# Optimization experiments

Measured on AMD Instinct MI355X. Metric: run time of the kernel, lower is better.

The kernel has to match this reference:

```python
import jax, jax.numpy as jnp
import numpy as np

B, S, SIZE = 2048, 512, 96  # size = embedding_size(32) * num_feature(3)


def setup_inputs() -> dict:
    key = jax.random.key(0)
    k1, k2, k3, k4, k5, k6, k7 = jax.random.split(key, 7)
    bound = 1.0 / np.sqrt(SIZE)  # nn.Linear default init range
    return {
        "seq_item_embedding": jax.random.normal(k1, (B, S, SIZE), dtype=jnp.float32),
        "target_item_embedding": jax.random.normal(k2, (B, 1, SIZE), dtype=jnp.float32),
        "mask": jax.random.randint(k3, (B, S + 1, 1), 0, 2).astype(jnp.bool_),
        "w1_weight": jax.random.uniform(k4, (SIZE, SIZE), jnp.float32, -bound, bound),
        "w1_bias": jax.random.uniform(k5, (SIZE,), jnp.float32, -bound, bound),
        "w2_weight": jax.random.uniform(k6, (SIZE, SIZE), jnp.float32, -bound, bound),
        "w2_bias": jax.random.uniform(k7, (SIZE,), jnp.float32, -bound, bound),
    }


def reference(seq_item_embedding, target_item_embedding, mask,
              w1_weight, w1_bias, w2_weight, w2_bias):
    # mask[:, :-1, :] -> [B, S] boolean (True = masked out)
    m = mask[:, :-1, 0]
    # w1(seq): [B, S, size]; note source reassigns seq_item_embedding to this,
    # so the final weighted pool uses the projected sequence.
    seq_h = jnp.einsum('bsd,ed->bse', seq_item_embedding, w1_weight) + w1_bias
    # w2(target): [B, 1, size], broadcasts over seq_len (repeat in torch)
    tgt_h = jnp.einsum('bqd,ed->bqe', target_item_embedding, w2_weight) + w2_bias
    # sigmoid(sum) reduced over feature dim -> scores [B, S]
    scores = jax.nn.sigmoid(seq_h + tgt_h).sum(axis=-1)
    scores = jnp.where(m, jnp.float32(-1e9), scores)
    attn = jax.nn.softmax(scores, axis=-1)  # [B, S]
    # weighted pool over seq dim -> [B, size]
    output = jnp.einsum('bs,bse->be', attn, seq_h)
    return output
```

## Files before the change

kernel.cpp:

```cpp
#include <hip/hip_runtime.h>
#include <hip/hip_bf16.h>
#include <math.h>

#define NB 2048
#define NS 512
#define ND 96
#define SH_STRIDE 112

typedef __attribute__((ext_vector_type(8))) short short8;
typedef __attribute__((ext_vector_type(4))) float floatx4;

__device__ __forceinline__ short f2bf(float f) {
    union { float f; unsigned u; } c; c.f = f;
    unsigned u = c.u;
    u += 0x7FFF + ((u >> 16) & 1);
    return (short)(u >> 16);
}
__device__ __forceinline__ float bf2f(short s) {
    union { unsigned u; float f; } c;
    c.u = ((unsigned)(unsigned short)s) << 16;
    return c.f;
}

__global__ __launch_bounds__(256, 1)
void attn_fused(const float* __restrict__ seq,
                const float* __restrict__ tgt,
                const int*   __restrict__ mask,
                const float* __restrict__ w1,
                const float* __restrict__ b1,
                const float* __restrict__ w2,
                const float* __restrict__ b2,
                float* __restrict__ out)
{
    __shared__ short sh[NS * SH_STRIDE];
    __shared__ float sc_lds[NS];
    __shared__ float attn[NS];
    __shared__ float tgt_h[ND];
    __shared__ float red[8];
    __shared__ float osum[2][ND];

    const int b    = blockIdx.x;
    const int tid  = threadIdx.x;
    const int lane = tid & 63;
    const int wave = tid >> 6;
    const int l15  = lane & 15;
    const int quad = lane >> 4;

    if (tid < ND) {
        const float* tv = tgt + (size_t)b * ND;
        const float* wr = w2 + tid * ND;
        float acc = b2[tid];
        #pragma unroll
        for (int d = 0; d < ND; d += 4) {
            acc += tv[d]*wr[d] + tv[d+1]*wr[d+1] + tv[d+2]*wr[d+2] + tv[d+3]*wr[d+3];
        }
        tgt_h[tid] = acc;
    }

    short8 bfrag[6][3];
    float biasv[6];
    #pragma unroll
    for (int t = 0; t < 6; ++t) {
        const int e = 16 * t + l15;
        biasv[t] = b1[e];
        #pragma unroll
        for (int kk = 0; kk < 3; ++kk) {
            const float* p = w1 + e * ND + kk * 32 + quad * 8;
            floatx4 p0 = *(const floatx4*)(p);
            floatx4 p1 = *(const floatx4*)(p + 4);
            short8 v;
            v[0]=f2bf(p0[0]); v[1]=f2bf(p0[1]); v[2]=f2bf(p0[2]); v[3]=f2bf(p0[3]);
            v[4]=f2bf(p1[0]); v[5]=f2bf(p1[1]); v[6]=f2bf(p1[2]); v[7]=f2bf(p1[3]);
            bfrag[t][kk] = v;
        }
    }

    __syncthreads();

    float tgtv[6];
    #pragma unroll
    for (int t = 0; t < 6; ++t) tgtv[t] = tgt_h[16 * t + l15];

    const float* abase = seq + ((size_t)b * NS + l15) * ND + quad * 8;

    #pragma unroll
    for (int sti = 0; sti < 8; ++sti) {
        const int st = wave * 8 + sti;
        const int s0 = st * 16;
        short8 af[3];
        #pragma unroll
        for (int kk = 0; kk < 3; ++kk) {
            const float* p = abase + (size_t)s0 * ND + kk * 32;
            floatx4 p0 = *(const floatx4*)(p);
            floatx4 p1 = *(const floatx4*)(p + 4);
            short8 v;
            v[0]=f2bf(p0[0]); v[1]=f2bf(p0[1]); v[2]=f2bf(p0[2]); v[3]=f2bf(p0[3]);
            v[4]=f2bf(p1[0]); v[5]=f2bf(p1[1]); v[6]=f2bf(p1[2]); v[7]=f2bf(p1[3]);
            af[kk] = v;
        }
        float part0 = 0.f, part1 = 0.f, part2 = 0.f, part3 = 0.f;
        #pragma unroll
        for (int t = 0; t < 6; ++t) {
            floatx4 acc = { biasv[t], biasv[t], biasv[t], biasv[t] };
            acc = __builtin_amdgcn_mfma_f32_16x16x32_bf16(af[0], bfrag[t][0], acc, 0, 0, 0);
            acc = __builtin_amdgcn_mfma_f32_16x16x32_bf16(af[1], bfrag[t][1], acc, 0, 0, 0);
            acc = __builtin_amdgcn_mfma_f32_16x16x32_bf16(af[2], bfrag[t][2], acc, 0, 0, 0);
            const int e = 16 * t + l15;
            short* dst = &sh[(s0 + quad * 4) * SH_STRIDE + e];
            const float x0 = acc[0], x1 = acc[1], x2 = acc[2], x3 = acc[3];
            dst[0]             = f2bf(x0);
            dst[SH_STRIDE]     = f2bf(x1);
            dst[2 * SH_STRIDE] = f2bf(x2);
            dst[3 * SH_STRIDE] = f2bf(x3);
            const float th = tgtv[t];
            part0 += 1.0f / (1.0f + __expf(-(x0 + th)));
            part1 += 1.0f / (1.0f + __expf(-(x1 + th)));
            part2 += 1.0f / (1.0f + __expf(-(x2 + th)));
            part3 += 1.0f / (1.0f + __expf(-(x3 + th)));
        }
        #pragma unroll
        for (int off = 1; off < 16; off <<= 1) {
            part0 += __shfl_xor(part0, off, 64);
            part1 += __shfl_xor(part1, off, 64);
            part2 += __shfl_xor(part2, off, 64);
            part3 += __shfl_xor(part3, off, 64);
        }
        if (l15 == 0) {
            sc_lds[s0 + quad * 4 + 0] = part0;
            sc_lds[s0 + quad * 4 + 1] = part1;
            sc_lds[s0 + quad * 4 + 2] = part2;
            sc_lds[s0 + quad * 4 + 3] = part3;
        }
    }
    __syncthreads();

    float v0 = sc_lds[tid];
    float v1 = sc_lds[tid + 256];
    if (mask[(size_t)b * (NS + 1) + tid] != 0)       v0 = -1e9f;
    if (mask[(size_t)b * (NS + 1) + tid + 256] != 0) v1 = -1e9f;
    float mx = fmaxf(v0, v1);
    #pragma unroll
    for (int off = 1; off < 64; off <<= 1) mx = fmaxf(mx, __shfl_xor(mx, off, 64));
    if (lane == 0) red[wave] = mx;
    __syncthreads();
    mx = fmaxf(fmaxf(red[0], red[1]), fmaxf(red[2], red[3]));
    const float e0 = __expf(v0 - mx);
    const float e1 = __expf(v1 - mx);
    float ssum = e0 + e1;
    #pragma unroll
    for (int off = 1; off < 64; off <<= 1) ssum += __shfl_xor(ssum, off, 64);
    if (lane == 0) red[4 + wave] = ssum;
    __syncthreads();
    const float inv = 1.0f / (red[4] + red[5] + red[6] + red[7]);
    attn[tid]       = e0 * inv;
    attn[tid + 256] = e1 * inv;
    __syncthreads();

    if (tid < 2 * ND) {
        const int half = tid / ND;
        const int e    = tid - half * ND;
        float acc = 0.f;
        const int sb = half * 256;
        #pragma unroll 4
        for (int s = sb; s < sb + 256; ++s) {
            acc += attn[s] * bf2f(sh[s * SH_STRIDE + e]);
        }
        osum[half][e] = acc;
    }
    __syncthreads();
    if (tid < ND) out[(size_t)b * ND + tid] = osum[0][tid] + osum[1][tid];
}

extern "C" void kernel_launch(void* const* d_in, const int* in_sizes, int n_in,
                              void* d_out, int out_size, void* d_ws, size_t ws_size,
                              hipStream_t stream) {
    const float* seq  = (const float*)d_in[0];
    const float* tgt  = (const float*)d_in[1];
    const int*   mask = (const int*)d_in[2];
    const float* w1   = (const float*)d_in[3];
    const float* b1   = (const float*)d_in[4];
    const float* w2   = (const float*)d_in[5];
    const float* b2   = (const float*)d_in[6];
    float* out = (float*)d_out;
    attn_fused<<<dim3(NB), dim3(256), 0, stream>>>(seq, tgt, mask, w1, b1, w2, b2, out);
}
```

Before: 637.8 us.

## Keep projected sequence in registers, stage W1 fragments in LDS, use 512 threads

The projected sequence is no longer written to a large bf16 LDS buffer (about 114KB, which allowed one block per CU). Each lane now keeps its MFMA outputs packed as bf16 pairs in registers and computes the weighted pool directly from them, using cross-quad shuffles and a per-wave LDS reduction. The W1 bf16 fragments move from per-thread registers into a small shared LDS table, and the block grows to 512 threads with launch bounds (512,4), so several blocks can be resident per CU for better latency hiding. The cost is extra LDS reads of W1 inside the MFMA loop and higher register pressure from the packed outputs.

Result: faster. 589.7 us (-7.5%).

```diff
diff --git a/kernel.cpp b/kernel.cpp
--- a/kernel.cpp
+++ b/kernel.cpp
@@ -1,28 +1,33 @@
 #include <hip/hip_runtime.h>
-#include <hip/hip_bf16.h>
 #include <math.h>
 
 #define NB 2048
 #define NS 512
 #define ND 96
-#define SH_STRIDE 112
 
 typedef __attribute__((ext_vector_type(8))) short short8;
 typedef __attribute__((ext_vector_type(4))) float floatx4;
 
-__device__ __forceinline__ short f2bf(float f) {
+__device__ __forceinline__ unsigned f2bfu(float f) {
     union { float f; unsigned u; } c; c.f = f;
     unsigned u = c.u;
     u += 0x7FFF + ((u >> 16) & 1);
-    return (short)(u >> 16);
-}
-__device__ __forceinline__ float bf2f(short s) {
-    union { unsigned u; float f; } c;
-    c.u = ((unsigned)(unsigned short)s) << 16;
-    return c.f;
-}
-
-__global__ __launch_bounds__(256, 1)
+    return u >> 16;
+}
+__device__ __forceinline__ unsigned pack2(float a, float b) {
+    return f2bfu(a) | (f2bfu(b) << 16);
+}
+__device__ __forceinline__ float lo_f(unsigned u) {
+    union { unsigned u; float f; } c; c.u = u << 16; return c.f;
+}
+__device__ __forceinline__ float hi_f(unsigned u) {
+    union { unsigned u; float f; } c; c.u = u & 0xFFFF0000u; return c.f;
+}
+__device__ __forceinline__ float sigm(float x) {
+    return 1.0f / (1.0f + __expf(-x));
+}
+
+__global__ __launch_bounds__(512, 4)
 void attn_fused(const float* __restrict__ seq,
                 const float* __restrict__ tgt,
                 const int*   __restrict__ mask,
@@ -32,12 +37,12 @@
                 const float* __restrict__ b2,
                 float* __restrict__ out)
 {
-    __shared__ short sh[NS * SH_STRIDE];
-    __shared__ float sc_lds[NS];
-    __shared__ float attn[NS];
-    __shared__ float tgt_h[ND];
-    __shared__ float red[8];
-    __shared__ float osum[2][ND];
+    __shared__ short w1f[18 * 64 * 8];
+    __shared__ float sc[NS];
+    __shared__ float at[NS];
+    __shared__ float th[ND];
+    __shared__ float red1[8], red2[8];
+    __shared__ float osum[8][ND];
 
     const int b    = blockIdx.x;
     const int tid  = threadIdx.x;
@@ -46,6 +51,23 @@
     const int l15  = lane & 15;
     const int quad = lane >> 4;
 
+    for (int idx = tid; idx < 1152; idx += 512) {
+        const int e  = idx / 12;
+        const int dc = idx - 12 * e;
+        const int kk = dc >> 2;
+        const int q  = dc & 3;
+        const float* p = w1 + e * ND + kk * 32 + q * 8;
+        floatx4 p0 = *(const floatx4*)(p);
+        floatx4 p1 = *(const floatx4*)(p + 4);
+        short8 v;
+        v[0]=(short)f2bfu(p0[0]); v[1]=(short)f2bfu(p0[1]);
+        v[2]=(short)f2bfu(p0[2]); v[3]=(short)f2bfu(p0[3]);
+        v[4]=(short)f2bfu(p1[0]); v[5]=(short)f2bfu(p1[1]);
+        v[6]=(short)f2bfu(p1[2]); v[7]=(short)f2bfu(p1[3]);
+        const int t = e >> 4, r = e & 15;
+        *(short8*)&w1f[(((t * 3 + kk) * 64) + q * 16 + r) * 8] = v;
+    }
+
     if (tid < ND) {
         const float* tv = tgt + (size_t)b * ND;
         const float* wr = w2 + tid * ND;
@@ -54,39 +76,23 @@
         for (int d = 0; d < ND; d += 4) {
             acc += tv[d]*wr[d] + tv[d+1]*wr[d+1] + tv[d+2]*wr[d+2] + tv[d+3]*wr[d+3];
         }
-        tgt_h[tid] = acc;
-    }
-
-    short8 bfrag[6][3];
-    float biasv[6];
+        th[tid] = acc;
+    }
+    __syncthreads();
+
+    float tgtv[6], biasv[6];
     #pragma unroll
     for (int t = 0; t < 6; ++t) {
-        const int e = 16 * t + l15;
-        biasv[t] = b1[e];
-        #pragma unroll
-        for (int kk = 0; kk < 3; ++kk) {
-            const float* p = w1 + e * ND + kk * 32 + quad * 8;
-            floatx4 p0 = *(const floatx4*)(p);
-            floatx4 p1 = *(const floatx4*)(p + 4);
-            short8 v;
-            v[0]=f2bf(p0[0]); v[1]=f2bf(p0[1]); v[2]=f2bf(p0[2]); v[3]=f2bf(p0[3]);
-            v[4]=f2bf(p1[0]); v[5]=f2bf(p1[1]); v[6]=f2bf(p1[2]); v[7]=f2bf(p1[3]);
-            bfrag[t][kk] = v;
-        }
-    }
-
-    __syncthreads();
-
-    float tgtv[6];
-    #pragma unroll
-    for (int t = 0; t < 6; ++t) tgtv[t] = tgt_h[16 * t + l15];
-
+        tgtv[t]  = th[16 * t + l15];
+        biasv[t] = b1[16 * t + l15];
+    }
+
+    unsigned pk[4][6][2];
     const float* abase = seq + ((size_t)b * NS + l15) * ND + quad * 8;
 
     #pragma unroll
-    for (int sti = 0; sti < 8; ++sti) {
-        const int st = wave * 8 + sti;
-        const int s0 = st * 16;
+    for (int sti = 0; sti < 4; ++sti) {
+        const int s0 = (wave * 4 + sti) * 16;
         short8 af[3];
         #pragma unroll
         for (int kk = 0; kk < 3; ++kk) {
@@ -94,81 +100,95 @@
             floatx4 p0 = *(const floatx4*)(p);
             floatx4 p1 = *(const floatx4*)(p + 4);
             short8 v;
-            v[0]=f2bf(p0[0]); v[1]=f2bf(p0[1]); v[2]=f2bf(p0[2]); v[3]=f2bf(p0[3]);
-            v[4]=f2bf(p1[0]); v[5]=f2bf(p1[1]); v[6]=f2bf(p1[2]); v[7]=f2bf(p1[3]);
+            v[0]=(short)f2bfu(p0[0]); v[1]=(short)f2bfu(p0[1]);
+            v[2]=(short)f2bfu(p0[2]); v[3]=(short)f2bfu(p0[3]);
+            v[4]=(short)f2bfu(p1[0]); v[5]=(short)f2bfu(p1[1]);
+            v[6]=(short)f2bfu(p1[2]); v[7]=(short)f2bfu(p1[3]);
             af[kk] = v;
         }
-        float part0 = 0.f, part1 = 0.f, part2 = 0.f, part3 = 0.f;
+        float p0s = 0.f, p1s = 0.f, p2s = 0.f, p3s = 0.f;
         #pragma unroll
         for (int t = 0; t < 6; ++t) {
             floatx4 acc = { biasv[t], biasv[t], biasv[t], biasv[t] };
-            acc = __builtin_amdgcn_mfma_f32_16x16x32_bf16(af[0], bfrag[t][0], acc, 0, 0, 0);
-            acc = __builtin_amdgcn_mfma_f32_16x16x32_bf16(af[1], bfrag[t][1], acc, 0, 0, 0);
-            acc = __builtin_amdgcn_mfma_f32_16x16x32_bf16(af[2], bfrag[t][2], acc, 0, 0, 0);
-            const int e = 16 * t + l15;
-            short* dst = &sh[(s0 + quad * 4) * SH_STRIDE + e];
-            const float x0 = acc[0], x1 = acc[1], x2 = acc[2], x3 = acc[3];
-            dst[0]             = f2bf(x0);
-            dst[SH_STRIDE]     = f2bf(x1);
-            dst[2 * SH_STRIDE] = f2bf(x2);
-            dst[3 * SH_STRIDE] = f2bf(x3);
-            const float th = tgtv[t];
-            part0 += 1.0f / (1.0f + __expf(-(x0 + th)));
-            part1 += 1.0f / (1.0f + __expf(-(x1 + th)));
-            part2 += 1.0f / (1.0f + __expf(-(x2 + th)));
-            part3 += 1.0f / (1.0f + __expf(-(x3 + th)));
+            #pragma unroll
+            for (int kk = 0; kk < 3; ++kk) {
+                const short8 bf = *(const short8*)&w1f[((t * 3 + kk) * 64 + lane) * 8];
+                acc = __builtin_amdgcn_mfma_f32_16x16x32_bf16(af[kk], bf, acc, 0, 0, 0);
+            }
+            pk[sti][t][0] = pack2(acc[0], acc[1]);
+            pk[sti][t][1] = pack2(acc[2], acc[3]);
+            const float thv = tgtv[t];
+            p0s += sigm(acc[0] + thv);
+            p1s += sigm(acc[1] + thv);
+            p2s += sigm(acc[2] + thv);
+            p3s += sigm(acc[3] + thv);
         }
         #pragma unroll
         for (int off = 1; off < 16; off <<= 1) {
-            part0 += __shfl_xor(part0, off, 64);
-            part1 += __shfl_xor(part1, off, 64);
-            part2 += __shfl_xor(part2, off, 64);
-            part3 += __shfl_xor(part3, off, 64);
+            p0s += __shfl_xor(p0s, off, 64);
+            p1s += __shfl_xor(p1s, off, 64);
+            p2s += __shfl_xor(p2s, off, 64);
+            p3s += __shfl_xor(p3s, off, 64);
         }
         if (l15 == 0) {
-            sc_lds[s0 + quad * 4 + 0] = part0;
-            sc_lds[s0 + quad * 4 + 1] = part1;
-            sc_lds[s0 + quad * 4 + 2] = part2;
-            sc_lds[s0 + quad * 4 + 3] = part3;
-        }
-    }
-    __syncthreads();
-
-    float v0 = sc_lds[tid];
-    float v1 = sc_lds[tid + 256];
-    if (mask[(size_t)b * (NS + 1) + tid] != 0)       v0 = -1e9f;
-    if (mask[(size_t)b * (NS + 1) + tid + 256] != 0) v1 = -1e9f;
-    float mx = fmaxf(v0, v1);
+            sc[s0 + quad * 4 + 0] = p0s;
+            sc[s0 + quad * 4 + 1] = p1s;
+            sc[s0 + quad * 4 + 2] = p2s;
+            sc[s0 + quad * 4 + 3] = p3s;
+        }
+    }
+    __syncthreads();
+
+    float v = sc[tid];
+    if (mask[(size_t)b * (NS + 1) + tid] != 0) v = -1e9f;
+    float mx = v;
     #pragma unroll
     for (int off = 1; off < 64; off <<= 1) mx = fmaxf(mx, __shfl_xor(mx, off, 64));
-    if (lane == 0) red[wave] = mx;
-    __syncthreads();
-    mx = fmaxf(fmaxf(red[0], red[1]), fmaxf(red[2], red[3]));
-    const float e0 = __expf(v0 - mx);
-    const float e1 = __expf(v1 - mx);
-    float ssum = e0 + e1;
+    if (lane == 0) red1[wave] = mx;
+    __syncthreads();
+    mx = red1[0];
+    #pragma unroll
+    for (int w = 1; w < 8; ++w) mx = fmaxf(mx, red1[w]);
+    const float e0 = __expf(v - mx);
+    float ssum = e0;
     #pragma unroll
     for (int off = 1; off < 64; off <<= 1) ssum += __shfl_xor(ssum, off, 64);
-    if (lane == 0) red[4 + wave] = ssum;
-    __syncthreads();
-    const float inv = 1.0f / (red[4] + red[5] + red[6] + red[7]);
-    attn[tid]       = e0 * inv;
-    attn[tid + 256] = e1 * inv;
-    __syncthreads();
-
-    if (tid < 2 * ND) {
-        const int half = tid / ND;
-        const int e    = tid - half * ND;
-        float acc = 0.f;
-        const int sb = half * 256;
-        #pragma unroll 4
-        for (int s = sb; s < sb + 256; ++s) {
-            acc += attn[s] * bf2f(sh[s * SH_STRIDE + e]);
-        }
-        osum[half][e] = acc;
-    }
-    __syncthreads();
-    if (tid < ND) out[(size_t)b * ND + tid] = osum[0][tid] + osum[1][tid];
+    if (lane == 0) red2[wave] = ssum;
+    __syncthreads();
+    float tot = red2[0];
+    #pragma unroll
+    for (int w = 1; w < 8; ++w) tot += red2[w];
+    at[tid] = e0 * (1.0f / tot);
+    __syncthreads();
+
+    float o[6] = {0.f, 0.f, 0.f, 0.f, 0.f, 0.f};
+    #pragma unroll
+    for (int sti = 0; sti < 4; ++sti) {
+        const int s0 = (wave * 4 + sti) * 16 + quad * 4;
+        const float a0 = at[s0], a1 = at[s0 + 1], a2 = at[s0 + 2], a3 = at[s0 + 3];
+        #pragma unroll
+        for (int t = 0; t < 6; ++t) {
+            const unsigned u0 = pk[sti][t][0];
+            const unsigned u1 = pk[sti][t][1];
+            o[t] += a0 * lo_f(u0) + a1 * hi_f(u0) + a2 * lo_f(u1) + a3 * hi_f(u1);
+        }
+    }
+    #pragma unroll
+    for (int t = 0; t < 6; ++t) {
+        o[t] += __shfl_xor(o[t], 16, 64);
+        o[t] += __shfl_xor(o[t], 32, 64);
+    }
+    if (quad == 0) {
+        #pragma unroll
+        for (int t = 0; t < 6; ++t) osum[wave][16 * t + l15] = o[t];
+    }
+    __syncthreads();
+    if (tid < ND) {
+        float a = 0.f;
+        #pragma unroll
+        for (int w = 0; w < 8; ++w) a += osum[w][tid];
+        out[(size_t)b * ND + tid] = a;
+    }
 }
 
 extern "C" void kernel_launch(void* const* d_in, const int* in_sizes, int n_in,
@@ -182,5 +202,5 @@
     const float* w2   = (const float*)d_in[5];
     const float* b2   = (const float*)d_in[6];
     float* out = (float*)d_out;
-    attn_fused<<<dim3(NB), dim3(256), 0, stream>>>(seq, tgt, mask, w1, b1, w2, b2, out);
-}
+    attn_fused<<<dim3(NB), dim3(512), 0, stream>>>(seq, tgt, mask, w1, b1, w2, b2, out);
+}
```
